# Optimization experiments

Measured on AMD Instinct MI355X. Metric: run time of the kernel, lower is better.

## Reference

```python
import jax, jax.numpy as jnp
import numpy as np

NUM_SEGMENT = 10
TIME_DURATION = 1.0
DT = TIME_DURATION / NUM_SEGMENT
N2 = 2
NUM_DATA = 2_000_000
HAM_MODEL = jnp.array([[0.0, 0.5], [0.5, 0.0]], dtype=jnp.complex64)  # 0.5 * sigma_x
TARGET_GATE = jnp.array([[0.0, 1.0], [1.0, 0.0]], dtype=jnp.complex64)  # sigma_x


def setup_inputs() -> dict:
    key = jax.random.key(0)
    k1, k2, k3 = jax.random.split(key, 3)
    para_ham_unknown = jax.random.uniform(k1, (N2, N2), jnp.float32, -0.1, 0.1)
    omega_data = jax.random.uniform(k2, (NUM_DATA, NUM_SEGMENT), jnp.float32, -0.1, 0.1)
    infedility_data = jax.random.uniform(k3, (NUM_DATA,), jnp.float32, 0.0, 0.1)
    return {"para_ham_unknown": para_ham_unknown, "omega_data": omega_data,
            "infedility_data": infedility_data}


def _real_matrix_to_hermitian(x):
    # symmetric real part + antisymmetric imaginary part -> Hermitian
    xc = x.astype(jnp.complex64)
    return (xc + xc.T) * 0.5 + 1j * (xc - xc.T) * 0.5


def reference(para_ham_unknown, omega_data, infedility_data):
    eye = jnp.eye(N2, dtype=jnp.complex64)
    herm = _real_matrix_to_hermitian(para_ham_unknown)
    ham_unknown = herm - jnp.trace(herm) * eye / N2  # traceless
    H = HAM_MODEL + ham_unknown                       # (2,2) Hermitian
    tr = jnp.trace(H)                                 # ~0 here, kept for generality
    H0 = H - tr * eye / N2                            # traceless part
    # For traceless 2x2 Hermitian H0: H0 @ H0 = r^2 I
    rsq = (jnp.einsum('ij,ji->', H0, H0).real) / N2
    r = jnp.sqrt(jnp.maximum(rsq, 1e-30))

    def step(unitary, omega_x):
        # closed-form: exp(-1j*phi*H) = e^{-i phi tr/2} (cos(phi r) I - i sin(phi r)/r H0)
        phi = DT * omega_x                            # (B,)
        theta = phi * r
        sinc = jnp.where(rsq > 1e-24, jnp.sin(theta) / r, phi)
        phase = jnp.exp(-1j * phi.astype(jnp.complex64) * tr / 2.0)
        u_step = phase[:, None, None] * (
            jnp.cos(theta).astype(jnp.complex64)[:, None, None] * eye
            - 1j * sinc.astype(jnp.complex64)[:, None, None] * H0)
        return jnp.einsum('bij,bjk->bik', u_step, unitary), None

    B = omega_data.shape[0]
    u0 = jnp.broadcast_to(eye, (B, N2, N2))
    unitary, _ = jax.lax.scan(step, u0, omega_data.T)  # scan over segments

    # tmp0[b] = trace(target_gate^H @ unitary[b])
    tmp0 = jnp.sum(TARGET_GATE.conj()[None, :, :] * unitary, axis=(1, 2))
    infidelity = 1.0 - (tmp0 * tmp0.conj()).real / (N2 * N2)
    loss = jnp.mean((infedility_data - infidelity) ** 2)
    return loss
```

## Files before the change

### kernel.cpp

```cpp
#include <hip/hip_runtime.h>


#define ND 2000000
#define NS 10
#define RPW 128
#define WPB 4
#define RPB (RPW * WPB)
#define PAD 11
#define WTILE (RPW * PAD)
#define GRID ((ND + RPB - 1) / RPB)

__global__ __launch_bounds__(256) void loss_kernel(
    const float* __restrict__ para,
    const float* __restrict__ omega,
    const float* __restrict__ infid,
    float* __restrict__ partial) {

    __shared__ float lds[WPB * WTILE];

    const float x00 = para[0], x01 = para[1], x10 = para[2], x11 = para[3];
    const float a  = 0.5f * (x00 - x11);
    const float cr = 0.5f + 0.5f * (x01 + x10);
    const float ci = 0.5f * (x01 - x10);
    const float r  = sqrtf(a * a + cr * cr + ci * ci);
    const float cr_over_r = cr / r;
    const float dt_r = 0.1f * r;

    const int tid  = threadIdx.x;
    const int lane = tid & 63;
    const int w    = tid >> 6;
    const unsigned rowW = (unsigned)blockIdx.x * RPB + (unsigned)w * RPW;
    const unsigned f2W  = rowW * 5u;
    float* wtile = &lds[w * WTILE];

    const float2* om2 = (const float2*)omega;
    #pragma unroll
    for (int k = 0; k < 10; ++k) {
        const unsigned fl  = 64u * k + (unsigned)lane;
        const unsigned idx = f2W + fl;
        float2 v = make_float2(0.0f, 0.0f);
        if (idx < (unsigned)(ND * 5)) v = om2[idx];
        const unsigned rl = fl / 5u;
        const unsigned p  = fl % 5u;
        const unsigned o  = rl * PAD + p * 2u;
        wtile[o]     = v.x;
        wtile[o + 1] = v.y;
    }
    __syncthreads();

    float acc = 0.0f;
    #pragma unroll
    for (int q = 0; q < 2; ++q) {
        const unsigned rl  = (unsigned)lane + 64u * q;
        const unsigned row = rowW + rl;
        if (row < (unsigned)ND) {
            const float* rp = &wtile[rl * PAD];
            float s = 0.0f;
            #pragma unroll
            for (int j = 0; j < 10; ++j) s += rp[j];
            const float theta = dt_r * s;
            const float t = cr_over_r * sinf(theta);
            const float inf_calc = 1.0f - t * t;
            const float d = infid[row] - inf_calc;
            acc += d * d;
        }
    }

    #pragma unroll
    for (int off = 32; off > 0; off >>= 1)
        acc += __shfl_down(acc, off, 64);

    __shared__ float wsum[WPB];
    if (lane == 0) wsum[w] = acc;
    __syncthreads();
    if (tid == 0) {
        partial[blockIdx.x] = wsum[0] + wsum[1] + wsum[2] + wsum[3];
    }
}

__global__ __launch_bounds__(256) void reduce_kernel(
    const float* __restrict__ partial,
    float* __restrict__ out) {

    const int tid = threadIdx.x;
    float acc = 0.0f;
    for (int i = tid; i < GRID; i += 256) acc += partial[i];

    #pragma unroll
    for (int off = 32; off > 0; off >>= 1)
        acc += __shfl_down(acc, off, 64);

    __shared__ float wsum[4];
    const int lane = tid & 63;
    const int w    = tid >> 6;
    if (lane == 0) wsum[w] = acc;
    __syncthreads();
    if (tid == 0)
        out[0] = (wsum[0] + wsum[1] + wsum[2] + wsum[3]) * (1.0f / (float)ND);
}

extern "C" void kernel_launch(void* const* d_in, const int* in_sizes, int n_in,
                              void* d_out, int out_size, void* d_ws, size_t ws_size,
                              hipStream_t stream) {
    const float* para  = (const float*)d_in[0];
    const float* omega = (const float*)d_in[1];
    const float* infid = (const float*)d_in[2];
    float* out     = (float*)d_out;
    float* partial = (float*)d_ws;

    loss_kernel<<<GRID, 256, 0, stream>>>(para, omega, infid, partial);
    reduce_kernel<<<1, 256, 0, stream>>>(partial, out);
}
```

Measured before the change: 133.6 us.

## Replace LDS-staged omega tiles with direct per-thread float4 loads of two rows

Drops the shared-memory transpose staging of omega. Each thread now loads two consecutive rows (20 floats) directly as five float4 loads, plus one float2 for the two infidelity values. This removes the LDS writes and reads and a barrier, and uses wider vector loads. In exchange, global loads within a wavefront are strided by 80 bytes per lane rather than fully coalesced.

```diff
diff --git a/kernel.cpp b/kernel.cpp
--- a/kernel.cpp
+++ b/kernel.cpp
@@ -2,12 +2,8 @@
 
 
 #define ND 2000000
-#define NS 10
-#define RPW 128
-#define WPB 4
-#define RPB (RPW * WPB)
-#define PAD 11
-#define WTILE (RPW * PAD)
+#define BLK 256
+#define RPB (2 * BLK)
 #define GRID ((ND + RPB - 1) / RPB)
 
 __global__ __launch_bounds__(256) void loss_kernel(
@@ -15,8 +11,6 @@
     const float* __restrict__ omega,
     const float* __restrict__ infid,
     float* __restrict__ partial) {
-
-    __shared__ float lds[WPB * WTILE];
 
     const float x00 = para[0], x01 = para[1], x10 = para[2], x11 = para[3];
     const float a  = 0.5f * (x00 - x11);
@@ -26,55 +20,43 @@
     const float cr_over_r = cr / r;
     const float dt_r = 0.1f * r;
 
-    const int tid  = threadIdx.x;
-    const int lane = tid & 63;
-    const int w    = tid >> 6;
-    const unsigned rowW = (unsigned)blockIdx.x * RPB + (unsigned)w * RPW;
-    const unsigned f2W  = rowW * 5u;
-    float* wtile = &lds[w * WTILE];
+    const unsigned tid  = (unsigned)blockIdx.x * BLK + threadIdx.x;
+    const unsigned row0 = tid * 2u;
+    float acc = 0.0f;
 
-    const float2* om2 = (const float2*)omega;
-    #pragma unroll
-    for (int k = 0; k < 10; ++k) {
-        const unsigned fl  = 64u * k + (unsigned)lane;
-        const unsigned idx = f2W + fl;
-        float2 v = make_float2(0.0f, 0.0f);
-        if (idx < (unsigned)(ND * 5)) v = om2[idx];
-        const unsigned rl = fl / 5u;
-        const unsigned p  = fl % 5u;
-        const unsigned o  = rl * PAD + p * 2u;
-        wtile[o]     = v.x;
-        wtile[o + 1] = v.y;
-    }
-    __syncthreads();
+    if (row0 < (unsigned)ND) {
+        const float4* p4 = (const float4*)omega + tid * 5u;
+        const float4 v0 = p4[0];
+        const float4 v1 = p4[1];
+        const float4 v2 = p4[2];
+        const float4 v3 = p4[3];
+        const float4 v4 = p4[4];
 
-    float acc = 0.0f;
-    #pragma unroll
-    for (int q = 0; q < 2; ++q) {
-        const unsigned rl  = (unsigned)lane + 64u * q;
-        const unsigned row = rowW + rl;
-        if (row < (unsigned)ND) {
-            const float* rp = &wtile[rl * PAD];
-            float s = 0.0f;
-            #pragma unroll
-            for (int j = 0; j < 10; ++j) s += rp[j];
-            const float theta = dt_r * s;
-            const float t = cr_over_r * sinf(theta);
-            const float inf_calc = 1.0f - t * t;
-            const float d = infid[row] - inf_calc;
-            acc += d * d;
-        }
+        const float s0 = ((v0.x + v0.y) + (v0.z + v0.w))
+                       + ((v1.x + v1.y) + (v1.z + v1.w)) + (v2.x + v2.y);
+        const float s1 = ((v2.z + v2.w) + (v3.x + v3.y))
+                       + ((v3.z + v3.w) + (v4.x + v4.y)) + (v4.z + v4.w);
+
+        const float2 fi = *((const float2*)infid + tid);
+
+        const float t0 = cr_over_r * sinf(dt_r * s0);
+        const float t1 = cr_over_r * sinf(dt_r * s1);
+        const float d0 = fi.x - (1.0f - t0 * t0);
+        const float d1 = fi.y - (1.0f - t1 * t1);
+        acc = d0 * d0 + d1 * d1;
     }
 
     #pragma unroll
     for (int off = 32; off > 0; off >>= 1)
         acc += __shfl_down(acc, off, 64);
 
-    __shared__ float wsum[WPB];
+    __shared__ float wsum[4];
+    const int lane = threadIdx.x & 63;
+    const int w    = threadIdx.x >> 6;
     if (lane == 0) wsum[w] = acc;
     __syncthreads();
-    if (tid == 0) {
-        partial[blockIdx.x] = wsum[0] + wsum[1] + wsum[2] + wsum[3];
+    if (threadIdx.x == 0) {
+        partial[blockIdx.x] = (wsum[0] + wsum[1]) + (wsum[2] + wsum[3]);
     }
 }
 
@@ -96,7 +78,7 @@
     if (lane == 0) wsum[w] = acc;
     __syncthreads();
     if (tid == 0)
-        out[0] = (wsum[0] + wsum[1] + wsum[2] + wsum[3]) * (1.0f / (float)ND);
+        out[0] = ((wsum[0] + wsum[1]) + (wsum[2] + wsum[3])) * (1.0f / (float)ND);
 }
 
 extern "C" void kernel_launch(void* const* d_in, const int* in_sizes, int n_in,
@@ -108,6 +90,6 @@
     float* out     = (float*)d_out;
     float* partial = (float*)d_ws;
 
-    loss_kernel<<<GRID, 256, 0, stream>>>(para, omega, infid, partial);
+    loss_kernel<<<GRID, BLK, 0, stream>>>(para, omega, infid, partial);
     reduce_kernel<<<1, 256, 0, stream>>>(partial, out);
 }
```

After: 124.9 us. 6.5% less time.
